# Kernel tuning notes

Measured on AMD Instinct MI355X. Metric: run time of the kernel, lower is better.

## Reference

```python
import jax, jax.numpy as jnp
import numpy as np

N_EMBED = 2048
N_HEAD = 16
HEAD_SIZE = N_EMBED // N_HEAD  # 128


def rotate_half(x):
    x1, x2 = jnp.split(x, 2, axis=-1)
    return jnp.concatenate((-x2, x1), axis=-1)


def setup_inputs() -> dict:
    key = jax.random.key(0)
    k_x, k_qkv, k_proj, k_b = jax.random.split(key, 4)
    B, T = 4, 2048
    x = jax.random.normal(k_x, (B, T, N_EMBED), dtype=jnp.float32)
    # weights stored as [in, out] so y = x @ W (equivalent param'n of nn.Linear)
    w_qkv = jax.random.normal(k_qkv, (N_EMBED, 3 * N_EMBED), dtype=jnp.float32) * (N_EMBED ** -0.5)
    w_proj = jax.random.normal(k_proj, (N_EMBED, N_EMBED), dtype=jnp.float32) * (N_EMBED ** -0.5)
    b_proj = jax.random.normal(k_b, (N_EMBED,), dtype=jnp.float32) * 0.02
    return {"x": x, "w_qkv": w_qkv, "w_proj": w_proj, "b_proj": b_proj}


def reference(x, w_qkv, w_proj, b_proj):
    B, T, C = x.shape
    H, D = N_HEAD, HEAD_SIZE
    qkv = x @ w_qkv                                   # [B,T,3C]
    q, k, v = jnp.split(qkv, 3, axis=2)
    q = q.reshape(B, T, H, D).transpose(0, 2, 1, 3)   # [B,H,T,D]
    k = k.reshape(B, T, H, D).transpose(0, 2, 1, 3)
    v = v.reshape(B, T, H, D).transpose(0, 2, 1, 3)
    # RoPE in fp32
    inv_freq = 1.0 / (10000.0 ** (jnp.arange(0, D, 2, dtype=jnp.float32) / D))
    t = jnp.arange(T, dtype=jnp.float32)
    freqs = jnp.einsum('i,j->ij', t, inv_freq)        # [T,D/2]
    emb = jnp.concatenate((freqs, freqs), axis=-1)    # [T,D]
    cos = jnp.cos(emb)[None, None, :, :]
    sin = jnp.sin(emb)[None, None, :, :]
    qf = q.astype(jnp.float32)
    kf = k.astype(jnp.float32)
    q = (qf * cos + rotate_half(qf) * sin).astype(v.dtype)
    k = (kf * cos + rotate_half(kf) * sin).astype(v.dtype)
    # causal SDPA
    scale = 1.0 / jnp.sqrt(jnp.asarray(D, dtype=q.dtype))
    scores = jnp.einsum('bhqd,bhkd->bhqk', q, k) * scale
    causal = jnp.tril(jnp.ones((T, T), dtype=bool))
    scores = jnp.where(causal[None, None, :, :], scores, jnp.finfo(scores.dtype).min)
    attn = jax.nn.softmax(scores, axis=-1)
    out = jnp.einsum('bhqk,bhkd->bhqd', attn, v)      # [B,H,T,D]
    out = out.transpose(0, 2, 1, 3).reshape(B, T, C)
    return out @ w_proj + b_proj
```

## Files before the change

kernel.cpp:

```cpp
#include <hip/hip_runtime.h>
#include <hip/hip_bf16.h>
#include <cstdint>
#include <cstddef>

typedef __bf16 bf16x8 __attribute__((ext_vector_type(8)));
typedef __bf16 bf16x4 __attribute__((ext_vector_type(4)));
typedef float  f32x4  __attribute__((ext_vector_type(4)));

__device__ __forceinline__ void lds_load16(const void* gsrc, void* ldst) {
    __builtin_amdgcn_global_load_lds(
        (const __attribute__((address_space(1))) unsigned int*)gsrc,
        (__attribute__((address_space(3))) unsigned int*)ldst,
        16, 0, 0);
}

__global__ __launch_bounds__(256) void cvt_k(const float* __restrict__ in,
                                             __bf16* __restrict__ out, int n8) {
    int i = blockIdx.x * 256 + threadIdx.x;
    if (i >= n8) return;
    const float4* p4 = (const float4*)in + (size_t)i * 2;
    float4 a = p4[0], b = p4[1];
    bf16x8 o;
    o[0] = (__bf16)a.x; o[1] = (__bf16)a.y; o[2] = (__bf16)a.z; o[3] = (__bf16)a.w;
    o[4] = (__bf16)b.x; o[5] = (__bf16)b.y; o[6] = (__bf16)b.z; o[7] = (__bf16)b.w;
    *((bf16x8*)out + i) = o;
}

__global__ __launch_bounds__(256) void transp_k(const float* __restrict__ W,
                                                __bf16* __restrict__ WT, int R, int C) {
    __shared__ float tile[32][33];
    int tx = threadIdx.x & 31, ty = threadIdx.x >> 5;
    int c0 = blockIdx.x * 32, r0 = blockIdx.y * 32;
#pragma unroll
    for (int k = 0; k < 4; ++k)
        tile[ty + 8 * k][tx] = W[(size_t)(r0 + ty + 8 * k) * C + c0 + tx];
    __syncthreads();
#pragma unroll
    for (int k = 0; k < 4; ++k)
        WT[(size_t)(c0 + ty + 8 * k) * R + r0 + tx] = (__bf16)tile[tx][ty + 8 * k];
}

__global__ __launch_bounds__(256) void sincos_k(float2* __restrict__ sc) {
    int idx = blockIdx.x * 256 + threadIdx.x;
    int t = idx >> 6, j = idx & 63;
    float inv = powf(10000.f, -(float)j / 64.f);
    float f = (float)t * inv;
    float s, c;
    sincosf(f, &s, &c);
    sc[idx] = make_float2(c, s);
}

__global__ __launch_bounds__(256) void rope_k(__bf16* __restrict__ qb, __bf16* __restrict__ kb,
                                              const float2* __restrict__ sc) {
    unsigned idx = blockIdx.x * 256 + threadIdx.x;
    int tensor = idx >> 20;
    unsigned i = idx & 0xFFFFFu;
    int jb = (i & 7) * 8;
    int t = (i >> 3) & 2047;
    int bh = i >> 14;
    __bf16* p = tensor ? kb : qb;
    size_t base = ((size_t)bh * 2048 + t) * 128;
    bf16x8 lo = *(bf16x8*)(p + base + jb);
    bf16x8 hi = *(bf16x8*)(p + base + 64 + jb);
    const float2* s2 = sc + t * 64 + jb;
    float scale = tensor ? 1.f : 0.08838834764831845f;
    bf16x8 olo, ohi;
#pragma unroll
    for (int e = 0; e < 8; ++e) {
        float c = s2[e].x, s = s2[e].y;
        float x1 = (float)lo[e], x2 = (float)hi[e];
        olo[e] = (__bf16)((x1 * c - x2 * s) * scale);
        ohi[e] = (__bf16)((x2 * c + x1 * s) * scale);
    }
    *(bf16x8*)(p + base + jb) = olo;
    *(bf16x8*)(p + base + 64 + jb) = ohi;
}

__global__ __launch_bounds__(512, 2) void gemm8_k(const __bf16* __restrict__ A,
                                                  const __bf16* __restrict__ Bt,
                                                  int nbn, int mode,
                                                  __bf16* __restrict__ qb, __bf16* __restrict__ kb,
                                                  __bf16* __restrict__ vt,
                                                  float* __restrict__ outp,
                                                  const float* __restrict__ bias) {
    __shared__ __bf16 lds[2][2][2][128 * 64];
    const int K = 2048, NT = K / 64;
    int nwg = gridDim.x;
    int per = nwg >> 3;
    int bid = blockIdx.x;
    int wg = (bid & 7) * per + (bid >> 3);
    int bm = wg / nbn, bn = wg % nbn;
    int m0 = bm * 256, n0 = bn * 256;
    int tid = threadIdx.x;
    int lane = tid & 63, wave = tid >> 6;
    int wm = wave >> 2, wn = wave & 3;
    int lr = lane & 15, lg = lane >> 4;

    f32x4 acc[8][4] = {};

    auto stageA = [&](int db, int sub, int kt) {
#pragma unroll
        for (int l = 0; l < 2; ++l) {
            int chunk = l * 512 + tid;
            int r = chunk >> 3, c16 = chunk & 7;
            int rg = m0 + ((r >> 6) << 7) + (sub << 6) + (r & 63);
            lds_load16(A + (size_t)rg * K + (kt << 6) + ((c16 ^ (r & 7)) << 3),
                       &lds[db][0][sub][chunk * 8]);
        }
    };
    auto stageB = [&](int db, int sub, int kt) {
#pragma unroll
        for (int l = 0; l < 2; ++l) {
            int chunk = l * 512 + tid;
            int r = chunk >> 3, c16 = chunk & 7;
            int rg = n0 + ((r >> 5) << 6) + (sub << 5) + (r & 31);
            lds_load16(Bt + (size_t)rg * K + (kt << 6) + ((c16 ^ (r & 7)) << 3),
                       &lds[db][1][sub][chunk * 8]);
        }
    };
    auto rdA = [&](int db, int sub, int q, int kk) -> bf16x8 {
        int r = (wm << 6) + (q << 4) + lr;
        int cb = ((kk << 6) + (lg << 4)) ^ ((r & 7) << 4);
        return *(const bf16x8*)((const char*)&lds[db][0][sub][0] + r * 128 + cb);
    };
    auto rdB = [&](int db, int j, int kk) -> bf16x8 {
        int sub = j >> 1;
        int r = (wn << 5) + ((j & 1) << 4) + lr;
        int cb = ((kk << 6) + (lg << 4)) ^ ((r & 7) << 4);
        return *(const bf16x8*)((const char*)&lds[db][1][sub][0] + r * 128 + cb);
    };

    stageA(0, 0, 0); stageB(0, 0, 0); stageB(0, 1, 0); stageA(0, 1, 0);
    asm volatile("s_waitcnt vmcnt(0)" ::: "memory");
    __builtin_amdgcn_s_barrier();

    bf16x8 a[4][2], b0[2][2], b1[2][2];
    for (int t = 0; t < NT; ++t) {
        int db = t & 1, dn = db ^ 1;
        bool pf = (t + 1 < NT);
#pragma unroll
        for (int q = 0; q < 4; ++q) { a[q][0] = rdA(db, 0, q, 0); a[q][1] = rdA(db, 0, q, 1); }
#pragma unroll
        for (int j = 0; j < 2; ++j) { b0[j][0] = rdB(db, j, 0); b0[j][1] = rdB(db, j, 1); }
        if (pf) stageA(dn, 0, t + 1);
        asm volatile("s_waitcnt vmcnt(4)" ::: "memory");
        __builtin_amdgcn_s_barrier();
        asm volatile("s_waitcnt lgkmcnt(0)" ::: "memory");
        __builtin_amdgcn_sched_barrier(0);
        __builtin_amdgcn_s_setprio(1);
#pragma unroll
        for (int q = 0; q < 4; ++q)
#pragma unroll
            for (int j = 0; j < 2; ++j)
#pragma unroll
                for (int kk = 0; kk < 2; ++kk)
                    acc[q][j] = __builtin_amdgcn_mfma_f32_16x16x32_bf16(a[q][kk], b0[j][kk], acc[q][j], 0, 0, 0);
        __builtin_amdgcn_s_setprio(0);
        __builtin_amdgcn_s_barrier();
#pragma unroll
        for (int j = 0; j < 2; ++j) { b1[j][0] = rdB(db, j + 2, 0); b1[j][1] = rdB(db, j + 2, 1); }
        if (pf) stageB(dn, 0, t + 1);
        asm volatile("s_waitcnt vmcnt(4)" ::: "memory");
        __builtin_amdgcn_s_barrier();
        asm volatile("s_waitcnt lgkmcnt(0)" ::: "memory");
        __builtin_amdgcn_sched_barrier(0);
        __builtin_amdgcn_s_setprio(1);
#pragma unroll
        for (int q = 0; q < 4; ++q)
#pragma unroll
            for (int j = 0; j < 2; ++j)
#pragma unroll
                for (int kk = 0; kk < 2; ++kk)
                    acc[q][j + 2] = __builtin_amdgcn_mfma_f32_16x16x32_bf16(a[q][kk], b1[j][kk], acc[q][j + 2], 0, 0, 0);
        __builtin_amdgcn_s_setprio(0);
        __builtin_amdgcn_s_barrier();
#pragma unroll
        for (int q = 0; q < 4; ++q) { a[q][0] = rdA(db, 1, q, 0); a[q][1] = rdA(db, 1, q, 1); }
        if (pf) stageB(dn, 1, t + 1);
        asm volatile("s_waitcnt vmcnt(4)" ::: "memory");
        __builtin_amdgcn_s_barrier();
        asm volatile("s_waitcnt lgkmcnt(0)" ::: "memory");
        __builtin_amdgcn_sched_barrier(0);
        __builtin_amdgcn_s_setprio(1);
#pragma unroll
        for (int q = 0; q < 4; ++q)
#pragma unroll
            for (int j = 0; j < 2; ++j)
#pragma unroll
                for (int kk = 0; kk < 2; ++kk)
                    acc[q + 4][j + 2] = __builtin_amdgcn_mfma_f32_16x16x32_bf16(a[q][kk], b1[j][kk], acc[q + 4][j + 2], 0, 0, 0);
        __builtin_amdgcn_s_setprio(0);
        __builtin_amdgcn_s_barrier();
        if (pf) stageA(dn, 1, t + 1);
        asm volatile("s_waitcnt vmcnt(4)" ::: "memory");
        __builtin_amdgcn_s_barrier();
        __builtin_amdgcn_sched_barrier(0);
        __builtin_amdgcn_s_setprio(1);
#pragma unroll
        for (int q = 0; q < 4; ++q)
#pragma unroll
            for (int j = 0; j < 2; ++j)
#pragma unroll
                for (int kk = 0; kk < 2; ++kk)
                    acc[q + 4][j] = __builtin_amdgcn_mfma_f32_16x16x32_bf16(a[q][kk], b0[j][kk], acc[q + 4][j], 0, 0, 0);
        __builtin_amdgcn_s_setprio(0);
        __builtin_amdgcn_s_barrier();
    }

    if (mode == 0) {
#pragma unroll
        for (int q = 0; q < 8; ++q) {
            int row_t = (wm << 7) + ((q >> 2) << 6) + ((q & 3) << 4) + (lg << 2);
#pragma unroll
            for (int j = 0; j < 4; ++j) {
                int c = n0 + (wn << 6) + (j << 4) + lr;
                int which = c >> 11;
                int h = (c & 2047) >> 7;
                int d = c & 127;
#pragma unroll
                for (int r = 0; r < 4; ++r) {
                    int row = m0 + row_t + r;
                    int b_ = row >> 11, tt = row & 2047;
                    __bf16 val = (__bf16)acc[q][j][r];
                    size_t bh = (size_t)(b_ * 16 + h);
                    if (which == 0)      qb[(bh * 2048 + tt) * 128 + d] = val;
                    else if (which == 1) kb[(bh * 2048 + tt) * 128 + d] = val;
                    else                 vt[(bh * 128 + d) * 2048 + tt] = val;
                }
            }
        }
    } else {
#pragma unroll
        for (int q = 0; q < 8; ++q) {
            int row_t = (wm << 7) + ((q >> 2) << 6) + ((q & 3) << 4) + (lg << 2);
#pragma unroll
            for (int j = 0; j < 4; ++j) {
                int col = n0 + (wn << 6) + (j << 4) + lr;
                float bv = bias[col];
#pragma unroll
                for (int r = 0; r < 4; ++r) {
                    int row = m0 + row_t + r;
                    outp[(size_t)row * 2048 + col] = acc[q][j][r] + bv;
                }
            }
        }
    }
}

__global__ __launch_bounds__(256, 2) void attn_k(const __bf16* __restrict__ qb,
                                                 const __bf16* __restrict__ kb,
                                                 const __bf16* __restrict__ vt,
                                                 __bf16* __restrict__ ao) {
    __shared__ __bf16 Ks[64 * 128];
    __shared__ __bf16 Vs[128 * 64];
    __shared__ __bf16 Ps[4][16 * 64];

    int bid = blockIdx.x;
    int qt = 31 - (bid >> 6);
    int bh = bid & 63;
    int qs = qt * 64;
    int tid = threadIdx.x, wave = tid >> 6, lane = tid & 63;
    int lr = lane & 15, lg = lane >> 4;

    bf16x8 qf[4];
    const __bf16* Qrow = qb + ((size_t)bh * 2048 + qs + wave * 16 + lr) * 128;
#pragma unroll
    for (int kk = 0; kk < 4; ++kk) qf[kk] = *(const bf16x8*)(Qrow + kk * 32 + lg * 8);

    f32x4 ot[8] = {};
    float m_run = -1e30f, l_run = 0.f;

    for (int ks = 0; ks <= qs; ks += 64) {
#pragma unroll
        for (int i = 0; i < 4; ++i) {
            int c = tid + i * 256;
            {
                int row = c >> 4;
                int cc = c ^ (row & 7);
                int dd = (cc & 15) * 8;
                lds_load16(kb + ((size_t)bh * 2048 + ks + row) * 128 + dd, Ks + c * 8);
            }
            {
                int row = c >> 3;
                int cc = c ^ (row & 7);
                int tt = (cc & 7) * 8;
                lds_load16(vt + ((size_t)bh * 128 + row) * 2048 + ks + tt, Vs + c * 8);
            }
        }
        __syncthreads();

        f32x4 st[4];
#pragma unroll
        for (int mt = 0; mt < 4; ++mt) {
            f32x4 s = {};
#pragma unroll
            for (int kk = 0; kk < 4; ++kk) {
                int row = mt * 16 + lr;
                const __bf16* kp = Ks + row * 128 + ((((kk * 64 + lg * 16)) ^ ((row & 7) << 4)) >> 1);
                bf16x8 afr = *(const bf16x8*)kp;
                s = __builtin_amdgcn_mfma_f32_16x16x32_bf16(afr, qf[kk], s, 0, 0, 0);
            }
            st[mt] = s;
        }

        if (ks == qs) {
            int q = qs + wave * 16 + lr;
#pragma unroll
            for (int mt = 0; mt < 4; ++mt)
#pragma unroll
                for (int r = 0; r < 4; ++r) {
                    int kv = ks + mt * 16 + lg * 4 + r;
                    if (kv > q) st[mt][r] = -1e30f;
                }
        }

        float pm = -1e30f;
#pragma unroll
        for (int mt = 0; mt < 4; ++mt)
#pragma unroll
            for (int r = 0; r < 4; ++r) pm = fmaxf(pm, st[mt][r]);
        pm = fmaxf(pm, __shfl_xor(pm, 16));
        pm = fmaxf(pm, __shfl_xor(pm, 32));
        float nm = fmaxf(m_run, pm);
        float alpha = __expf(m_run - nm);
        float psum = 0.f;
#pragma unroll
        for (int mt = 0; mt < 4; ++mt)
#pragma unroll
            for (int r = 0; r < 4; ++r) {
                float p = __expf(st[mt][r] - nm);
                psum += p;
                st[mt][r] = p;
            }
        psum += __shfl_xor(psum, 16);
        psum += __shfl_xor(psum, 32);
        l_run = l_run * alpha + psum;
        m_run = nm;
#pragma unroll
        for (int t8 = 0; t8 < 8; ++t8) ot[t8] *= alpha;

#pragma unroll
        for (int mt = 0; mt < 4; ++mt) {
            bf16x4 pk;
#pragma unroll
            for (int r = 0; r < 4; ++r) pk[r] = (__bf16)st[mt][r];
            int byteoff = lr * 128 + (((mt * 32 + lg * 8)) ^ ((lr & 7) << 4));
            *(bf16x4*)((char*)&Ps[wave][0] + byteoff) = pk;
        }

        bf16x8 pfr[2];
#pragma unroll
        for (int kk = 0; kk < 2; ++kk) {
            const char* pp = (const char*)&Ps[wave][0] + lr * 128 + (((kk * 64 + lg * 16)) ^ ((lr & 7) << 4));
            pfr[kk] = *(const bf16x8*)pp;
        }
#pragma unroll
        for (int dt = 0; dt < 8; ++dt) {
#pragma unroll
            for (int kk = 0; kk < 2; ++kk) {
                int row = dt * 16 + lr;
                const __bf16* vp = Vs + row * 64 + ((((kk * 64 + lg * 16)) ^ ((row & 7) << 4)) >> 1);
                bf16x8 afr = *(const bf16x8*)vp;
                ot[dt] = __builtin_amdgcn_mfma_f32_16x16x32_bf16(afr, pfr[kk], ot[dt], 0, 0, 0);
            }
        }
        __syncthreads();
    }

    float inv = 1.f / l_run;
    int b_ = bh >> 4, h = bh & 15;
    size_t rowbase = ((size_t)b_ * 2048 + qs + wave * 16 + lr) * 2048 + h * 128;
#pragma unroll
    for (int dt = 0; dt < 8; ++dt) {
        bf16x4 o;
#pragma unroll
        for (int r = 0; r < 4; ++r) o[r] = (__bf16)(ot[dt][r] * inv);
        *(bf16x4*)(ao + rowbase + dt * 16 + lg * 4) = o;
    }
}

extern "C" void kernel_launch(void* const* d_in, const int* in_sizes, int n_in,
                              void* d_out, int out_size, void* d_ws, size_t ws_size,
                              hipStream_t stream) {
    const float* x      = (const float*)d_in[0];
    const float* w_qkv  = (const float*)d_in[1];
    const float* w_proj = (const float*)d_in[2];
    const float* b_proj = (const float*)d_in[3];
    float* out = (float*)d_out;
    char* ws = (char*)d_ws;

    __bf16* xb  = (__bf16*)(ws);
    __bf16* wqt = (__bf16*)(ws + 33554432);
    __bf16* wpt = (__bf16*)(ws + 58720256);
    __bf16* qb  = (__bf16*)(ws + 67108864);
    __bf16* kb  = (__bf16*)(ws + 100663296);
    __bf16* vt  = (__bf16*)(ws + 134217728);
    __bf16* ao  = (__bf16*)(ws + 167772160);
    float2* sc  = (float2*)(ws + 201326592);

    hipLaunchKernelGGL(cvt_k, dim3(8192), dim3(256), 0, stream, x, xb, 2097152);
    hipLaunchKernelGGL(transp_k, dim3(192, 64), dim3(256), 0, stream, w_qkv, wqt, 2048, 6144);
    hipLaunchKernelGGL(transp_k, dim3(64, 64), dim3(256), 0, stream, w_proj, wpt, 2048, 2048);
    hipLaunchKernelGGL(sincos_k, dim3(512), dim3(256), 0, stream, sc);
    hipLaunchKernelGGL(gemm8_k, dim3(768), dim3(512), 0, stream,
                       xb, wqt, 24, 0, qb, kb, vt, (float*)nullptr, (const float*)nullptr);
    hipLaunchKernelGGL(rope_k, dim3(8192), dim3(256), 0, stream, qb, kb, sc);
    hipLaunchKernelGGL(attn_k, dim3(2048), dim3(256), 0, stream, qb, kb, vt, ao);
    hipLaunchKernelGGL(gemm8_k, dim3(256), dim3(512), 0, stream,
                       ao, wpt, 8, 1, (__bf16*)nullptr, (__bf16*)nullptr, (__bf16*)nullptr,
                       out, b_proj);
}
```

Baseline: 453.2 us.

## Reorder GEMM mainloop to issue all next-tile prefetches early, split by k-half

The GEMM mainloop now issues all four global-to-LDS prefetches for the next K tile at the start of each iteration. It then splits the MFMA phases by k-half rather than by N-subtile, using separate fragment registers for each half, with vmcnt waits placed partway through and at the end of the iteration. The goal is a longer window between issuing global loads and waiting on them. The attention kernel also raises wave priority around its MFMA blocks. The new vmcnt counts depend on exact load-issue ordering and could race if the counts are wrong.

```diff
diff --git a/kernel.cpp b/kernel.cpp
--- a/kernel.cpp
+++ b/kernel.cpp
@@ -131,19 +131,18 @@
     };
 
     stageA(0, 0, 0); stageB(0, 0, 0); stageB(0, 1, 0); stageA(0, 1, 0);
-    asm volatile("s_waitcnt vmcnt(0)" ::: "memory");
+    asm volatile("s_waitcnt vmcnt(2)" ::: "memory");
     __builtin_amdgcn_s_barrier();
 
-    bf16x8 a[4][2], b0[2][2], b1[2][2];
+    bf16x8 a[4], a2[4], b[4], b2[4];
     for (int t = 0; t < NT; ++t) {
         int db = t & 1, dn = db ^ 1;
         bool pf = (t + 1 < NT);
 #pragma unroll
-        for (int q = 0; q < 4; ++q) { a[q][0] = rdA(db, 0, q, 0); a[q][1] = rdA(db, 0, q, 1); }
-#pragma unroll
-        for (int j = 0; j < 2; ++j) { b0[j][0] = rdB(db, j, 0); b0[j][1] = rdB(db, j, 1); }
-        if (pf) stageA(dn, 0, t + 1);
-        asm volatile("s_waitcnt vmcnt(4)" ::: "memory");
+        for (int q = 0; q < 4; ++q) a[q] = rdA(db, 0, q, 0);
+#pragma unroll
+        for (int j = 0; j < 4; ++j) b[j] = rdB(db, j, 0);
+        if (pf) { stageA(dn, 0, t + 1); stageB(dn, 0, t + 1); stageB(dn, 1, t + 1); stageA(dn, 1, t + 1); }
         __builtin_amdgcn_s_barrier();
         asm volatile("s_waitcnt lgkmcnt(0)" ::: "memory");
         __builtin_amdgcn_sched_barrier(0);
@@ -151,16 +150,14 @@
 #pragma unroll
         for (int q = 0; q < 4; ++q)
 #pragma unroll
-            for (int j = 0; j < 2; ++j)
-#pragma unroll
-                for (int kk = 0; kk < 2; ++kk)
-                    acc[q][j] = __builtin_amdgcn_mfma_f32_16x16x32_bf16(a[q][kk], b0[j][kk], acc[q][j], 0, 0, 0);
-        __builtin_amdgcn_s_setprio(0);
-        __builtin_amdgcn_s_barrier();
-#pragma unroll
-        for (int j = 0; j < 2; ++j) { b1[j][0] = rdB(db, j + 2, 0); b1[j][1] = rdB(db, j + 2, 1); }
-        if (pf) stageB(dn, 0, t + 1);
-        asm volatile("s_waitcnt vmcnt(4)" ::: "memory");
+            for (int j = 0; j < 4; ++j)
+                acc[q][j] = __builtin_amdgcn_mfma_f32_16x16x32_bf16(a[q], b[j], acc[q][j], 0, 0, 0);
+        __builtin_amdgcn_s_setprio(0);
+        __builtin_amdgcn_s_barrier();
+#pragma unroll
+        for (int q = 0; q < 4; ++q) a2[q] = rdA(db, 0, q, 1);
+#pragma unroll
+        for (int j = 0; j < 4; ++j) b2[j] = rdB(db, j, 1);
         __builtin_amdgcn_s_barrier();
         asm volatile("s_waitcnt lgkmcnt(0)" ::: "memory");
         __builtin_amdgcn_sched_barrier(0);
@@ -168,16 +165,14 @@
 #pragma unroll
         for (int q = 0; q < 4; ++q)
 #pragma unroll
-            for (int j = 0; j < 2; ++j)
-#pragma unroll
-                for (int kk = 0; kk < 2; ++kk)
-                    acc[q][j + 2] = __builtin_amdgcn_mfma_f32_16x16x32_bf16(a[q][kk], b1[j][kk], acc[q][j + 2], 0, 0, 0);
-        __builtin_amdgcn_s_setprio(0);
-        __builtin_amdgcn_s_barrier();
-#pragma unroll
-        for (int q = 0; q < 4; ++q) { a[q][0] = rdA(db, 1, q, 0); a[q][1] = rdA(db, 1, q, 1); }
-        if (pf) stageB(dn, 1, t + 1);
-        asm volatile("s_waitcnt vmcnt(4)" ::: "memory");
+            for (int j = 0; j < 4; ++j)
+                acc[q][j] = __builtin_amdgcn_mfma_f32_16x16x32_bf16(a2[q], b2[j], acc[q][j], 0, 0, 0);
+        __builtin_amdgcn_s_setprio(0);
+        if (pf) asm volatile("s_waitcnt vmcnt(8)" ::: "memory");
+        else    asm volatile("s_waitcnt vmcnt(0)" ::: "memory");
+        __builtin_amdgcn_s_barrier();
+#pragma unroll
+        for (int q = 0; q < 4; ++q) a[q] = rdA(db, 1, q, 0);
         __builtin_amdgcn_s_barrier();
         asm volatile("s_waitcnt lgkmcnt(0)" ::: "memory");
         __builtin_amdgcn_sched_barrier(0);
@@ -185,25 +180,23 @@
 #pragma unroll
         for (int q = 0; q < 4; ++q)
 #pragma unroll
-            for (int j = 0; j < 2; ++j)
-#pragma unroll
-                for (int kk = 0; kk < 2; ++kk)
-                    acc[q + 4][j + 2] = __builtin_amdgcn_mfma_f32_16x16x32_bf16(a[q][kk], b1[j][kk], acc[q + 4][j + 2], 0, 0, 0);
-        __builtin_amdgcn_s_setprio(0);
-        __builtin_amdgcn_s_barrier();
-        if (pf) stageA(dn, 1, t + 1);
-        asm volatile("s_waitcnt vmcnt(4)" ::: "memory");
-        __builtin_amdgcn_s_barrier();
+            for (int j = 0; j < 4; ++j)
+                acc[q + 4][j] = __builtin_amdgcn_mfma_f32_16x16x32_bf16(a[q], b[j], acc[q + 4][j], 0, 0, 0);
+        __builtin_amdgcn_s_setprio(0);
+        __builtin_amdgcn_s_barrier();
+#pragma unroll
+        for (int q = 0; q < 4; ++q) a2[q] = rdA(db, 1, q, 1);
+        __builtin_amdgcn_s_barrier();
+        asm volatile("s_waitcnt lgkmcnt(0)" ::: "memory");
         __builtin_amdgcn_sched_barrier(0);
         __builtin_amdgcn_s_setprio(1);
 #pragma unroll
         for (int q = 0; q < 4; ++q)
 #pragma unroll
-            for (int j = 0; j < 2; ++j)
-#pragma unroll
-                for (int kk = 0; kk < 2; ++kk)
-                    acc[q + 4][j] = __builtin_amdgcn_mfma_f32_16x16x32_bf16(a[q][kk], b0[j][kk], acc[q + 4][j], 0, 0, 0);
-        __builtin_amdgcn_s_setprio(0);
+            for (int j = 0; j < 4; ++j)
+                acc[q + 4][j] = __builtin_amdgcn_mfma_f32_16x16x32_bf16(a2[q], b2[j], acc[q + 4][j], 0, 0, 0);
+        __builtin_amdgcn_s_setprio(0);
+        if (pf) asm volatile("s_waitcnt vmcnt(2)" ::: "memory");
         __builtin_amdgcn_s_barrier();
     }
 
@@ -290,6 +283,7 @@
         __syncthreads();
 
         f32x4 st[4];
+        __builtin_amdgcn_s_setprio(1);
 #pragma unroll
         for (int mt = 0; mt < 4; ++mt) {
             f32x4 s = {};
@@ -302,6 +296,7 @@
             }
             st[mt] = s;
         }
+        __builtin_amdgcn_s_setprio(0);
 
         if (ks == qs) {
             int q = qs + wave * 16 + lr;
@@ -354,6 +349,7 @@
             const char* pp = (const char*)&Ps[wave][0] + lr * 128 + (((kk * 64 + lg * 16)) ^ ((lr & 7) << 4));
             pfr[kk] = *(const bf16x8*)pp;
         }
+        __builtin_amdgcn_s_setprio(1);
 #pragma unroll
         for (int dt = 0; dt < 8; ++dt) {
 #pragma unroll
@@ -364,6 +360,7 @@
                 ot[dt] = __builtin_amdgcn_mfma_f32_16x16x32_bf16(afr, pfr[kk], ot[dt], 0, 0, 0);
             }
         }
+        __builtin_amdgcn_s_setprio(0);
         __syncthreads();
     }
 
```

Measured after the change: 468.1 us. +3.3%, slower.
